# Kernel tuning notes

Hardware: AMD Instinct MI355X
Metric: run time of the kernel (lower is better)

The kernel has to match this reference:

```python
import jax, jax.numpy as jnp
import numpy as np

HIDDEN = 1024
HEADS = 16
HEAD_DIM = HIDDEN // HEADS


def setup_inputs() -> dict:
    key = jax.random.key(0)
    ks = jax.random.split(key, 7)
    B, S, H = 8, 1024, HIDDEN
    hidden_states = jax.random.normal(ks[0], (B, S, H), dtype=jnp.float32)
    attention_mask = jnp.zeros((B, 1, 1, S), dtype=jnp.float32)
    # Xavier-uniform weights [out, in], zero biases (matches module init)
    limit = float(np.sqrt(6.0 / (H + H)))
    Wq = jax.random.uniform(ks[1], (H, H), minval=-limit, maxval=limit, dtype=jnp.float32)
    Wk = jax.random.uniform(ks[2], (H, H), minval=-limit, maxval=limit, dtype=jnp.float32)
    Wv = jax.random.uniform(ks[3], (H, H), minval=-limit, maxval=limit, dtype=jnp.float32)
    bq = jnp.zeros((H,), dtype=jnp.float32)
    bk = jnp.zeros((H,), dtype=jnp.float32)
    bv = jnp.zeros((H,), dtype=jnp.float32)
    return {"hidden_states": hidden_states, "attention_mask": attention_mask,
            "Wq": Wq, "bq": bq, "Wk": Wk, "bk": bk, "Wv": Wv, "bv": bv}


def _split_heads(x):
    # [B, S, H] -> [B, heads, S, head_dim]
    B, S, _ = x.shape
    return x.reshape(B, S, HEADS, HEAD_DIM).transpose(0, 2, 1, 3)


def reference(hidden_states, attention_mask, Wq, bq, Wk, bk, Wv, bv):
    # Linear projections: y = x @ W^T + b  (weights stored [out, in] as in torch)
    q = _split_heads(hidden_states @ Wq.T + bq)
    k = _split_heads(hidden_states @ Wk.T + bk)
    v = _split_heads(hidden_states @ Wv.T + bv)
    scale = 1.0 / (HEAD_DIM ** 0.5)
    scores = jnp.einsum('bhqd,bhkd->bhqk', q, k) * scale  # [B,heads,S,S]
    scores = scores + attention_mask
    probs = jax.nn.softmax(scores, axis=-1)
    # dropout is identity at inference
    ctx = jnp.einsum('bhqk,bhkd->bhqd', probs, v)
    B, _, S, _ = ctx.shape
    return ctx.transpose(0, 2, 1, 3).reshape(B, S, HIDDEN)
```

## Files before the change

### kernel.cpp

```cpp
#include <hip/hip_runtime.h>
#include <hip/hip_bf16.h>
#include <stdint.h>

#define B_ 8
#define S_ 1024
#define NH_ 16
#define D_ 64
#define H_ 1024
#define M_TOT (B_*S_)
#define LOG2E 1.44269504088896f

typedef __attribute__((ext_vector_type(8))) short short8;
typedef __attribute__((ext_vector_type(4))) float f32x4;
typedef __attribute__((ext_vector_type(16))) float f32x16;

#if __has_builtin(__builtin_amdgcn_exp2f)
#define EXP2(x) __builtin_amdgcn_exp2f(x)
#else
#define EXP2(x) __expf((x) * 0.69314718056f)
#endif

static __device__ __forceinline__ unsigned short f2bf(float f) {
  union { float f; unsigned u; } c; c.f = f;
  unsigned u = c.u;
  return (unsigned short)((u + 0x7fffu + ((u >> 16) & 1u)) >> 16);
}

static __device__ __forceinline__ void gld_lds16(void* lds, const void* g) {
  __builtin_amdgcn_global_load_lds((const __attribute__((address_space(1))) unsigned*)g,
                                   (__attribute__((address_space(3))) unsigned*)lds, 16, 0, 0);
}

#define WAIT_LGKM(n)  asm volatile("s_waitcnt lgkmcnt(" #n ")" ::: "memory")
#define WAIT_VM(n)    asm volatile("s_waitcnt vmcnt(" #n ")" ::: "memory")
#define SBAR()        __builtin_amdgcn_s_barrier()
#define SCHED0()      __builtin_amdgcn_sched_barrier(0)
#define PRIO1()       __builtin_amdgcn_s_setprio(1)
#define PRIO0()       __builtin_amdgcn_s_setprio(0)

__global__ void cvt_f32_bf16(const float* __restrict__ X,
                             const float* __restrict__ Wq,
                             const float* __restrict__ Wk,
                             const float* __restrict__ Wv,
                             unsigned short* __restrict__ Xbf,
                             unsigned short* __restrict__ Wbf) {
  const long long NX = (long long)M_TOT * H_;
  const long long NW = (long long)H_ * H_;
  long long t = (long long)blockIdx.x * blockDim.x + threadIdx.x;
  const long long stride = (long long)gridDim.x * blockDim.x;
  const long long total4 = (NX + 3 * NW) >> 2;
  for (; t < total4; t += stride) {
    long long e = t << 2;
    const float* src; unsigned short* dst;
    if (e < NX) { src = X + e; dst = Xbf + e; }
    else {
      long long r = e - NX;
      int w = (int)(r / NW);
      long long o = r - (long long)w * NW;
      src = (w == 0 ? Wq : (w == 1 ? Wk : Wv)) + o;
      dst = Wbf + (long long)w * NW + o;
    }
    float4 v = *(const float4*)src;
    ushort4 u;
    u.x = f2bf(v.x); u.y = f2bf(v.y); u.z = f2bf(v.z); u.w = f2bf(v.w);
    *(ushort4*)dst = u;
  }
}

#define QBM 256
#define QBN 256
#define QBK 64
#define ABYTES 32768
#define BUFSZ  65536

#define MMQ(I0, J0, AF, BF)                                               \
  _Pragma("unroll")                                                       \
  for (int a_ = 0; a_ < 4; ++a_)                                          \
    _Pragma("unroll")                                                     \
    for (int b_ = 0; b_ < 2; ++b_)                                        \
      _Pragma("unroll")                                                   \
      for (int k_ = 0; k_ < 2; ++k_)                                      \
        acc[(I0) + a_][(J0) + b_] = __builtin_amdgcn_mfma_f32_16x16x32_bf16( \
            AF[a_][k_], BF[b_][k_], acc[(I0) + a_][(J0) + b_], 0, 0, 0);

#define RD_A4(DST, FI0, BUF)                                              \
  _Pragma("unroll")                                                       \
  for (int f_ = 0; f_ < 4; ++f_)                                          \
    _Pragma("unroll")                                                     \
    for (int k_ = 0; k_ < 2; ++k_) DST[f_][k_] = rdA(BUF, (FI0) + f_, k_);

#define RD_B2(DST, FI0, BUF)                                              \
  _Pragma("unroll")                                                       \
  for (int f_ = 0; f_ < 2; ++f_)                                          \
    _Pragma("unroll")                                                     \
    for (int k_ = 0; k_ < 2; ++k_) DST[f_][k_] = rdB(BUF, (FI0) + f_, k_);

__global__ __launch_bounds__(512, 1) void qkv_gemm(
    const unsigned short* __restrict__ Xbf,
    const unsigned short* __restrict__ Wbf,
    const float* __restrict__ bq, const float* __restrict__ bk,
    const float* __restrict__ bv,
    unsigned short* __restrict__ Qo, unsigned short* __restrict__ Ko,
    unsigned short* __restrict__ Vt) {
  __shared__ char lds[2 * BUFSZ];

  const int tid = threadIdx.x;
  const int w = tid >> 6;
  const int l = tid & 63;
  const int lrow = l & 15, lgrp = l >> 4;
  const int wm = w >> 2, wn = w & 3;

  const int orig = blockIdx.x;
  const int xcd = orig & 7;
  const int slot = orig >> 3;
  const int nz = slot >> 2;
  const int mtile = (xcd * 4 + (slot & 3)) * QBM;
  const int ntile = (nz & 3) * QBN;
  const int z = nz >> 2;

  const unsigned short* Wz = Wbf + (long long)z * H_ * H_;

  const int srow = l >> 3;
  const int sslot = l & 7;
  auto stageA = [&](char* buf, int j, int k0) {
    int row = j * 8 + srow;
    int so = (sslot ^ (row & 7)) * 8;
    gld_lds16(buf + j * 1024, Xbf + (long long)(mtile + row) * H_ + k0 + so);
  };
  auto stageB = [&](char* buf, int j, int k0) {
    int row = j * 8 + srow;
    int so = (sslot ^ (row & 7)) * 8;
    gld_lds16(buf + ABYTES + j * 1024, Wz + (long long)(ntile + row) * H_ + k0 + so);
  };

  const int strA = wm * 128;
  const int strB = wn * 64;
  const int offA = (z == 2) ? ABYTES : 0;
  const int offB = (z == 2) ? 0 : ABYTES;
  auto rdA = [&](const char* buf, int fi, int ks) -> short8 {
    int r = strA + fi * 16 + lrow;
    return *(const short8*)(buf + offA + r * 128 + (((ks * 4 + lgrp) ^ (r & 7)) * 16));
  };
  auto rdB = [&](const char* buf, int fi, int ks) -> short8 {
    int r = strB + fi * 16 + lrow;
    return *(const short8*)(buf + offB + r * 128 + (((ks * 4 + lgrp) ^ (r & 7)) * 16));
  };

  f32x4 acc[8][4];
  f32x4 zero = {0.f, 0.f, 0.f, 0.f};
  #pragma unroll
  for (int a = 0; a < 8; ++a)
    #pragma unroll
    for (int c = 0; c < 4; ++c) acc[a][c] = zero;

  short8 a0[4][2], a1[4][2], b0[2][2], b1[2][2];

  #pragma unroll
  for (int c = 0; c < 4; ++c) stageA(lds, w * 4 + c, 0);
  #pragma unroll
  for (int c = 0; c < 4; ++c) stageB(lds, w * 4 + c, 0);
  SCHED0(); WAIT_VM(0); SCHED0();
  SBAR();
  RD_A4(a0, 0, lds);
  RD_B2(b0, 0, lds);

  #pragma unroll 1
  for (int t = 0; t < 16; ++t) {
    char* buf  = lds + ((t & 1) ? BUFSZ : 0);
    char* nbuf = lds + ((t & 1) ? 0 : BUFSZ);
    const bool st = (t < 15);
    const int k0n = (t + 1) * QBK;

    if (st) {
      stageA(nbuf, w * 4 + 0, k0n); stageA(nbuf, w * 4 + 1, k0n);
      stageA(nbuf, w * 4 + 2, k0n); stageA(nbuf, w * 4 + 3, k0n);
      stageB(nbuf, w * 4 + 0, k0n); stageB(nbuf, w * 4 + 1, k0n);
      stageB(nbuf, w * 4 + 2, k0n); stageB(nbuf, w * 4 + 3, k0n);
    }

    RD_A4(a1, 4, buf);
    SCHED0(); WAIT_LGKM(8); SCHED0();
    PRIO1(); MMQ(0, 0, a0, b0); PRIO0();

    RD_B2(b1, 2, buf);
    SCHED0(); WAIT_LGKM(4); SCHED0();
    PRIO1(); MMQ(4, 0, a1, b0); PRIO0();

    SCHED0(); WAIT_LGKM(0); SCHED0();
    PRIO1(); MMQ(4, 2, a1, b1); PRIO0();

    PRIO1(); MMQ(0, 2, a0, b1); PRIO0();

    if (st) { SCHED0(); WAIT_VM(0); SCHED0(); }
    SBAR();
    if (st) {
      RD_A4(a0, 0, nbuf);
      RD_B2(b0, 0, nbuf);
    }
  }

  const float* bias = (z == 0) ? bq : (z == 1) ? bk : bv;
  if (z != 2) {
    unsigned short* O = (z == 0) ? Qo : Ko;
    #pragma unroll
    for (int in = 0; in < 4; ++in) {
      int n = ntile + wn * 64 + in * 16 + lrow;
      float bv_ = bias[n];
      int h = n >> 6, d = n & 63;
      #pragma unroll
      for (int im = 0; im < 8; ++im)
        #pragma unroll
        for (int r = 0; r < 4; ++r) {
          int m = mtile + wm * 128 + im * 16 + lgrp * 4 + r;
          float val = acc[im][in][r] + bv_;
          if (z == 0) val *= 0.125f * LOG2E;
          int b = m >> 10, s = m & 1023;
          O[(((long long)(b * NH_ + h)) * S_ + s) * D_ + d] = f2bf(val);
        }
    }
  } else {
    #pragma unroll
    for (int im = 0; im < 8; ++im)
      #pragma unroll
      for (int r = 0; r < 4; ++r) {
        int nfull = ntile + wm * 128 + im * 16 + lgrp * 4 + r;
        float bv_ = bias[nfull];
        int h = nfull >> 6, d = nfull & 63;
        #pragma unroll
        for (int in = 0; in < 4; ++in) {
          int mfull = mtile + wn * 64 + in * 16 + lrow;
          float val = acc[im][in][r] + bv_;
          int b = mfull >> 10, s = mfull & 1023;
          Vt[(((long long)(b * NH_ + h)) * D_ + d) * S_ + s] = f2bf(val);
        }
      }
  }
}

__global__ __launch_bounds__(256, 2) void attn_fused(
    const unsigned short* __restrict__ Qbf,
    const unsigned short* __restrict__ Kbf,
    const unsigned short* __restrict__ Vtb,
    const float* __restrict__ mask,
    float* __restrict__ out) {
  __shared__ char lds[32768];
  const int tid = threadIdx.x, w = tid >> 6, l = tid & 63;
  const int l31 = l & 31, h = l >> 5;

  const int lid = blockIdx.x;
  const int xcd = lid & 7, k8 = lid >> 3;
  const int bh = xcd * 16 + (k8 >> 2);
  const int qt = k8 & 3;
  const int b = bh >> 4, hd = bh & 15;
  const int q0 = qt * 256 + w * 64;

  const unsigned short* Kg = Kbf + (long long)bh * S_ * D_;
  const unsigned short* Vg = Vtb + (long long)bh * D_ * S_;
  const float* mrow = mask + b * S_;

  {
    const int row = (w * 2) * 8 + (l >> 3);
    const int row1 = (w * 2 + 1) * 8 + (l >> 3);
    const int so = ((l & 7) ^ (row & 7)) * 8;
    const int so1 = ((l & 7) ^ (row1 & 7)) * 8;
    gld_lds16(lds + (w * 2) * 1024,        Kg + (long long)row * D_ + so);
    gld_lds16(lds + (w * 2 + 1) * 1024,    Kg + (long long)row1 * D_ + so1);
    gld_lds16(lds + 8192 + (w * 2) * 1024, Vg + (long long)row * S_ + so);
    gld_lds16(lds + 8192 + (w * 2 + 1) * 1024, Vg + (long long)row1 * S_ + so1);
  }

  short8 qf[2][4];
  #pragma unroll
  for (int qb = 0; qb < 2; ++qb)
    #pragma unroll
    for (int ks = 0; ks < 4; ++ks)
      qf[qb][ks] = *(const short8*)(Qbf + ((long long)bh * S_ + q0 + qb * 32 + l31) * D_ + ks * 16 + 8 * h);

  f32x16 acc[2][2];
  #pragma unroll
  for (int db = 0; db < 2; ++db)
    #pragma unroll
    for (int qb = 0; qb < 2; ++qb)
      #pragma unroll
      for (int r = 0; r < 16; ++r) acc[db][qb][r] = 0.f;
  float m_run[2] = {-1e30f, -1e30f};
  float l_run[2] = {0.f, 0.f};

  __syncthreads();

  for (int kt = 0; kt < S_ / 64; ++kt) {
    const int p = kt & 1;
    char* ldsK = lds + p * 16384;
    char* ldsV = ldsK + 8192;
    const int key0 = kt * 64;

    if (kt < S_ / 64 - 1) {
      char* nb = lds + (p ^ 1) * 16384;
      const int nk0 = key0 + 64;
      #pragma unroll
      for (int t = 0; t < 2; ++t) {
        int j = w * 2 + t;
        int row = j * 8 + (l >> 3);
        int so = ((l & 7) ^ (row & 7)) * 8;
        gld_lds16(nb + j * 1024,        Kg + (long long)(nk0 + row) * D_ + so);
        gld_lds16(nb + 8192 + j * 1024, Vg + (long long)row * S_ + nk0 + so);
      }
    }

    f32x16 sc[2][2];
    #pragma unroll
    for (int kb = 0; kb < 2; ++kb)
      #pragma unroll
      for (int qb = 0; qb < 2; ++qb)
        #pragma unroll
        for (int r = 0; r < 16; ++r) sc[kb][qb][r] = 0.f;

    #pragma unroll
    for (int kb = 0; kb < 2; ++kb) {
      short8 kf[4];
      #pragma unroll
      for (int ks = 0; ks < 4; ++ks) {
        int row = kb * 32 + l31;
        int g = (2 * ks + h) ^ (row & 7);
        kf[ks] = *(const short8*)(ldsK + row * 128 + g * 16);
      }
      __builtin_amdgcn_s_setprio(1);
      #pragma unroll
      for (int qb = 0; qb < 2; ++qb)
        #pragma unroll
        for (int ks = 0; ks < 4; ++ks)
          sc[kb][qb] = __builtin_amdgcn_mfma_f32_32x32x16_bf16(
              kf[ks], qf[qb][ks], sc[kb][qb], 0, 0, 0);
      __builtin_amdgcn_s_setprio(0);
    }

    short8 pfrag[2][4];
    #pragma unroll
    for (int qb = 0; qb < 2; ++qb) {
      float sv[32];
      #pragma unroll
      for (int kb = 0; kb < 2; ++kb)
        #pragma unroll
        for (int rg = 0; rg < 4; ++rg) {
          f32x4 m4 = *(const f32x4*)(mrow + key0 + kb * 32 + rg * 8 + 4 * h);
          #pragma unroll
          for (int c = 0; c < 4; ++c)
            sv[kb * 16 + rg * 4 + c] = fmaf(m4[c], LOG2E, sc[kb][qb][rg * 4 + c]);
        }
      float r16[16];
      #pragma unroll
      for (int i = 0; i < 16; ++i) r16[i] = fmaxf(sv[i], sv[i + 16]);
      #pragma unroll
      for (int i = 0; i < 8; ++i) r16[i] = fmaxf(r16[i], r16[i + 8]);
      #pragma unroll
      for (int i = 0; i < 4; ++i) r16[i] = fmaxf(r16[i], r16[i + 4]);
      float pm = fmaxf(fmaxf(r16[0], r16[1]), fmaxf(r16[2], r16[3]));
      pm = fmaxf(pm, __shfl_xor(pm, 32));
      if (!__all(pm - m_run[qb] <= 11.5f)) {
        float mn = fmaxf(m_run[qb], pm);
        float rs = EXP2(m_run[qb] - mn);
        m_run[qb] = mn;
        l_run[qb] *= rs;
        #pragma unroll
        for (int db = 0; db < 2; ++db)
          #pragma unroll
          for (int r = 0; r < 16; ++r) acc[db][qb][r] *= rs;
      }
      const float mcur = m_run[qb];
      #pragma unroll
      for (int i = 0; i < 32; ++i) sv[i] = EXP2(sv[i] - mcur);
      #pragma unroll
      for (int i = 0; i < 16; ++i) r16[i] = sv[i] + sv[i + 16];
      #pragma unroll
      for (int i = 0; i < 8; ++i) r16[i] = r16[i] + r16[i + 8];
      #pragma unroll
      for (int i = 0; i < 4; ++i) r16[i] = r16[i] + r16[i + 4];
      float ps = (r16[0] + r16[1]) + (r16[2] + r16[3]);
      ps += __shfl_xor(ps, 32);
      l_run[qb] += ps;

      unsigned Wd[8][2];
      #pragma unroll
      for (int j = 0; j < 8; ++j) {
        int base = (j >> 2) * 16 + (j & 3) * 4;
        asm("v_cvt_pk_bf16_f32 %0, %1, %2" : "=v"(Wd[j][0]) : "v"(sv[base + 0]), "v"(sv[base + 1]));
        asm("v_cvt_pk_bf16_f32 %0, %1, %2" : "=v"(Wd[j][1]) : "v"(sv[base + 2]), "v"(sv[base + 3]));
      }
      #pragma unroll
      for (int ks = 0; ks < 4; ++ks) {
        unsigned s0 = h ? Wd[2 * ks][0] : Wd[2 * ks + 1][0];
        unsigned s1 = h ? Wd[2 * ks][1] : Wd[2 * ks + 1][1];
        unsigned r0 = __shfl_xor(s0, 32);
        unsigned r1 = __shfl_xor(s1, 32);
        unsigned o0 = h ? Wd[2 * ks + 1][0] : Wd[2 * ks][0];
        unsigned o1 = h ? Wd[2 * ks + 1][1] : Wd[2 * ks][1];
        union { unsigned u[4]; short8 s; } fu;
        fu.u[0] = h ? r0 : o0;
        fu.u[1] = h ? r1 : o1;
        fu.u[2] = h ? o0 : r0;
        fu.u[3] = h ? o1 : r1;
        pfrag[qb][ks] = fu.s;
      }
    }

    #pragma unroll
    for (int db = 0; db < 2; ++db) {
      short8 vf[4];
      #pragma unroll
      for (int ks = 0; ks < 4; ++ks) {
        int row = db * 32 + l31;
        int g = (2 * ks + h) ^ (row & 7);
        vf[ks] = *(const short8*)(ldsV + row * 128 + g * 16);
      }
      __builtin_amdgcn_s_setprio(1);
      #pragma unroll
      for (int qb = 0; qb < 2; ++qb)
        #pragma unroll
        for (int ks = 0; ks < 4; ++ks)
          acc[db][qb] = __builtin_amdgcn_mfma_f32_32x32x16_bf16(
              vf[ks], pfrag[qb][ks], acc[db][qb], 0, 0, 0);
      __builtin_amdgcn_s_setprio(0);
    }

    __syncthreads();
  }

  #pragma unroll
  for (int qb = 0; qb < 2; ++qb) {
    float inv = 1.0f / l_run[qb];
    int q = q0 + qb * 32 + l31;
    float* orow = out + ((long long)b * S_ + q) * H_ + hd * D_;
    #pragma unroll
    for (int db = 0; db < 2; ++db)
      #pragma unroll
      for (int rg = 0; rg < 4; ++rg) {
        f32x4 v4;
        #pragma unroll
        for (int c = 0; c < 4; ++c) v4[c] = acc[db][qb][rg * 4 + c] * inv;
        *(f32x4*)(orow + db * 32 + rg * 8 + 4 * h) = v4;
      }
  }
}

extern "C" void kernel_launch(void* const* d_in, const int* in_sizes, int n_in,
                              void* d_out, int out_size, void* d_ws, size_t ws_size,
                              hipStream_t stream) {
  const float* X    = (const float*)d_in[0];
  const float* mask = (const float*)d_in[1];
  const float* Wq   = (const float*)d_in[2];
  const float* bq   = (const float*)d_in[3];
  const float* Wk   = (const float*)d_in[4];
  const float* bk   = (const float*)d_in[5];
  const float* Wv   = (const float*)d_in[6];
  const float* bv   = (const float*)d_in[7];
  float* out = (float*)d_out;

  char* ws = (char*)d_ws;
  unsigned short* Xbf = (unsigned short*)ws;
  unsigned short* Wbf = (unsigned short*)(ws + 16777216);
  unsigned short* Qb  = (unsigned short*)(ws + 23068672);
  unsigned short* Kb  = (unsigned short*)(ws + 39845888);
  unsigned short* Vt  = (unsigned short*)(ws + 56623104);

  hipLaunchKernelGGL(cvt_f32_bf16, dim3(2048), dim3(256), 0, stream,
                     X, Wq, Wk, Wv, Xbf, Wbf);
  hipLaunchKernelGGL(qkv_gemm, dim3(384), dim3(512), 0, stream,
                     Xbf, Wbf, bq, bk, bv, Qb, Kb, Vt);
  hipLaunchKernelGGL(attn_fused, dim3(512), dim3(256), 0, stream,
                     Qb, Kb, Vt, mask, out);
}
```

Baseline: 135.5 us.

## Restructure QKV GEMM main loop into barrier-synchronized four-phase ping-pong schedule

Replaces the register double-buffered fragment prefetch (a0/a1, b0/b1 with partial lgkmcnt waits) in the QKV GEMM inner loop with a four-phase schedule. Each phase issues LDS fragment reads, interleaves part of the global->LDS staging, then waits fully and runs a quarter of the MFMAs, with block barriers around each MFMA cluster. This cuts live fragment registers (one A set instead of two) and tries to get waves to alternate memory and MFMA work in lockstep. It adds more barriers and removes the cross-iteration fragment prefetch, so LDS read latency may be exposed more often.

```diff
diff --git a/kernel.cpp b/kernel.cpp
--- a/kernel.cpp
+++ b/kernel.cpp
@@ -31,7 +31,7 @@
                                    (__attribute__((address_space(3))) unsigned*)lds, 16, 0, 0);
 }
 
-#define WAIT_LGKM(n)  asm volatile("s_waitcnt lgkmcnt(" #n ")" ::: "memory")
+#define WAIT_LGKM0()  asm volatile("s_waitcnt lgkmcnt(0)" ::: "memory")
 #define WAIT_VM(n)    asm volatile("s_waitcnt vmcnt(" #n ")" ::: "memory")
 #define SBAR()        __builtin_amdgcn_s_barrier()
 #define SCHED0()      __builtin_amdgcn_sched_barrier(0)
@@ -83,17 +83,17 @@
         acc[(I0) + a_][(J0) + b_] = __builtin_amdgcn_mfma_f32_16x16x32_bf16( \
             AF[a_][k_], BF[b_][k_], acc[(I0) + a_][(J0) + b_], 0, 0, 0);
 
-#define RD_A4(DST, FI0, BUF)                                              \
+#define RD_A(BUF, MH)                                                     \
   _Pragma("unroll")                                                       \
   for (int f_ = 0; f_ < 4; ++f_)                                          \
     _Pragma("unroll")                                                     \
-    for (int k_ = 0; k_ < 2; ++k_) DST[f_][k_] = rdA(BUF, (FI0) + f_, k_);
-
-#define RD_B2(DST, FI0, BUF)                                              \
+    for (int k_ = 0; k_ < 2; ++k_) A[f_][k_] = rdA(BUF, MH, f_, k_);
+
+#define RD_B(DST, BUF, NH)                                                \
   _Pragma("unroll")                                                       \
   for (int f_ = 0; f_ < 2; ++f_)                                          \
     _Pragma("unroll")                                                     \
-    for (int k_ = 0; k_ < 2; ++k_) DST[f_][k_] = rdB(BUF, (FI0) + f_, k_);
+    for (int k_ = 0; k_ < 2; ++k_) DST[f_][k_] = rdB(BUF, NH, f_, k_);
 
 __global__ __launch_bounds__(512, 1) void qkv_gemm(
     const unsigned short* __restrict__ Xbf,
@@ -133,16 +133,14 @@
     gld_lds16(buf + ABYTES + j * 1024, Wz + (long long)(ntile + row) * H_ + k0 + so);
   };
 
-  const int strA = wm * 128;
-  const int strB = wn * 64;
   const int offA = (z == 2) ? ABYTES : 0;
   const int offB = (z == 2) ? 0 : ABYTES;
-  auto rdA = [&](const char* buf, int fi, int ks) -> short8 {
-    int r = strA + fi * 16 + lrow;
+  auto rdA = [&](const char* buf, int mh, int fi, int ks) -> short8 {
+    int r = wm * 128 + mh * 64 + fi * 16 + lrow;
     return *(const short8*)(buf + offA + r * 128 + (((ks * 4 + lgrp) ^ (r & 7)) * 16));
   };
-  auto rdB = [&](const char* buf, int fi, int ks) -> short8 {
-    int r = strB + fi * 16 + lrow;
+  auto rdB = [&](const char* buf, int nh, int fi, int ks) -> short8 {
+    int r = wn * 64 + nh * 32 + fi * 16 + lrow;
     return *(const short8*)(buf + offB + r * 128 + (((ks * 4 + lgrp) ^ (r & 7)) * 16));
   };
 
@@ -153,7 +151,7 @@
     #pragma unroll
     for (int c = 0; c < 4; ++c) acc[a][c] = zero;
 
-  short8 a0[4][2], a1[4][2], b0[2][2], b1[2][2];
+  short8 A[4][2], B0[2][2], B1[2][2];
 
   #pragma unroll
   for (int c = 0; c < 4; ++c) stageA(lds, w * 4 + c, 0);
@@ -161,8 +159,6 @@
   for (int c = 0; c < 4; ++c) stageB(lds, w * 4 + c, 0);
   SCHED0(); WAIT_VM(0); SCHED0();
   SBAR();
-  RD_A4(a0, 0, lds);
-  RD_B2(b0, 0, lds);
 
   #pragma unroll 1
   for (int t = 0; t < 16; ++t) {
@@ -171,32 +167,36 @@
     const bool st = (t < 15);
     const int k0n = (t + 1) * QBK;
 
+    RD_A(buf, 0);
+    RD_B(B0, buf, 0);
     if (st) {
       stageA(nbuf, w * 4 + 0, k0n); stageA(nbuf, w * 4 + 1, k0n);
       stageA(nbuf, w * 4 + 2, k0n); stageA(nbuf, w * 4 + 3, k0n);
+    }
+    SBAR();
+    WAIT_LGKM0(); SCHED0();
+    PRIO1(); MMQ(0, 0, A, B0); PRIO0();
+    SBAR();
+
+    RD_B(B1, buf, 1);
+    if (st) {
       stageB(nbuf, w * 4 + 0, k0n); stageB(nbuf, w * 4 + 1, k0n);
       stageB(nbuf, w * 4 + 2, k0n); stageB(nbuf, w * 4 + 3, k0n);
     }
-
-    RD_A4(a1, 4, buf);
-    SCHED0(); WAIT_LGKM(8); SCHED0();
-    PRIO1(); MMQ(0, 0, a0, b0); PRIO0();
-
-    RD_B2(b1, 2, buf);
-    SCHED0(); WAIT_LGKM(4); SCHED0();
-    PRIO1(); MMQ(4, 0, a1, b0); PRIO0();
-
-    SCHED0(); WAIT_LGKM(0); SCHED0();
-    PRIO1(); MMQ(4, 2, a1, b1); PRIO0();
-
-    PRIO1(); MMQ(0, 2, a0, b1); PRIO0();
-
+    SBAR();
+    WAIT_LGKM0(); SCHED0();
+    PRIO1(); MMQ(0, 2, A, B1); PRIO0();
+    SBAR();
+
+    RD_A(buf, 1);
+    SBAR();
+    WAIT_LGKM0(); SCHED0();
+    PRIO1(); MMQ(4, 2, A, B1); PRIO0();
+    SBAR();
+
+    PRIO1(); MMQ(4, 0, A, B0); PRIO0();
     if (st) { SCHED0(); WAIT_VM(0); SCHED0(); }
     SBAR();
-    if (st) {
-      RD_A4(a0, 0, nbuf);
-      RD_B2(b0, 0, nbuf);
-    }
   }
 
   const float* bias = (z == 0) ? bq : (z == 1) ? bk : bv;
```

Measured after the change: 138.2 us. Within noise of the previous version (+2.0%).
